# Performance work log

Hardware: AMD Instinct MI355X
Metric: run time of the kernel (lower is better)

Reference implementation:

```python
import jax, jax.numpy as jnp
import numpy as np

K = 5          # reassembly kernel size
S = 2          # scale factor
ENC_PAD = 1    # encoder_kernel_size // 2


def _conv2d(x, w, pad):
    return jax.lax.conv_general_dilated(
        x, w, window_strides=(1, 1), padding=[(pad, pad), (pad, pad)],
        dimension_numbers=('NCHW', 'OIHW', 'NCHW'))


def setup_inputs() -> dict:
    key = jax.random.key(0)
    k1, k2, k3 = jax.random.split(key, 3)
    x = jax.random.normal(k1, (2, 256, 40, 40), dtype=jnp.float32)
    # channel compressor: xavier-uniform-ish 1x1 conv weight (64, 256, 1, 1)
    limit = np.sqrt(6.0 / (256 + 64)).astype(np.float32)
    w_comp = jax.random.uniform(k2, (64, 256, 1, 1), dtype=jnp.float32,
                                minval=-limit, maxval=limit)
    # content encoder: normal(0, 0.001), out = k^2*s^2 = 100 channels
    w_enc = 0.001 * jax.random.normal(k3, (100, 64, 3, 3), dtype=jnp.float32)
    return {"x": x, "w_comp": w_comp, "w_enc": w_enc}


def reference(x, w_comp, w_enc):
    b, c, h, w = x.shape
    k2 = K * K
    h_up, w_up = h * S, w * S

    # --- kernel prediction ---
    compressed = _conv2d(x, w_comp, 0)                # (b, 64, h, w)
    kern = _conv2d(compressed, w_enc, ENC_PAD)        # (b, k2*S^2, h, w)
    # pixel shuffle: (b, k2, S, S, h, w) -> (b, k2, h, S, w, S) -> (b, k2, h_up, w_up)
    kern = kern.reshape(b, k2, S, S, h, w).transpose(0, 1, 4, 2, 5, 3)
    kern = kern.reshape(b, k2, h_up * w_up)
    kern = jax.nn.softmax(kern, axis=1)               # softmax over k2

    # --- unfold (im2col, padding K//2) ---
    pad = K // 2
    xp = jnp.pad(x, ((0, 0), (0, 0), (pad, pad), (pad, pad)))
    # (b, c, k2, h, w): channel-major, kernel offsets inner (matches torch F.unfold)
    patches = jnp.stack([xp[:, :, i:i + h, j:j + w]
                         for i in range(K) for j in range(K)], axis=2)
    x_unfold = patches.reshape(b, c, k2, h * w)

    # --- reassembly (faithful to the torch 'efficient' path) ---
    # torch repeat_interleaves x_unfold S^2 times along the h*w axis and
    # multiplies with kernels flattened in (h_up*w_up) row-major order; that
    # pairing is exactly kern reshaped to (b, k2, h*w, S^2):
    kern4 = kern.reshape(b, k2, h * w, S * S)
    out = jnp.einsum('bckp,bkpd->bcpd', x_unfold, kern4)  # (b, c, h*w, S^2)
    return out.reshape(b, c, h_up, w_up)
```

## Files before the change

### kernel.cpp

```cpp
#include <hip/hip_runtime.h>

#define B   2
#define C   256
#define CM  64
#define CE  100
#define H   40
#define W   40
#define HW  1600
#define KK  25

__global__ __launch_bounds__(256) void k1_conv1x1(
    const float* __restrict__ x, const float* __restrict__ w,
    float* __restrict__ pc) {
  const int t = blockIdx.x, ich = blockIdx.y, b = blockIdx.z;
  __shared__ __align__(16) float xs[64 * 64];
  __shared__ __align__(16) float wsA[64 * 64];
  const int tid = threadIdx.x;

  const float4* x4 = (const float4*)(x + ((size_t)b * C + ich * 64) * HW + t * 64);
#pragma unroll
  for (int i = 0; i < 4; i++) {
    int idx = tid + i * 256;
    ((float4*)xs)[idx] = x4[(idx >> 4) * 400 + (idx & 15)];
  }
  const float4* w4 = (const float4*)w;
#pragma unroll
  for (int i = 0; i < 4; i++) {
    int idx = tid + i * 256;
    int icq = idx >> 6, oc = idx & 63;
    float4 f = w4[oc * 64 + ich * 16 + icq];
    wsA[(icq * 4 + 0) * 64 + oc] = f.x;
    wsA[(icq * 4 + 1) * 64 + oc] = f.y;
    wsA[(icq * 4 + 2) * 64 + oc] = f.z;
    wsA[(icq * 4 + 3) * 64 + oc] = f.w;
  }
  __syncthreads();

  const int ty = tid >> 4, tx = tid & 15;
  float acc[4][4];
#pragma unroll
  for (int i = 0; i < 4; i++)
#pragma unroll
    for (int j = 0; j < 4; j++) acc[i][j] = 0.f;

#pragma unroll 4
  for (int icl = 0; icl < 64; icl++) {
    float4 a = *(const float4*)&wsA[icl * 64 + ty * 4];
    float4 bb = *(const float4*)&xs[icl * 64 + tx * 4];
    float av[4] = {a.x, a.y, a.z, a.w};
    float bv[4] = {bb.x, bb.y, bb.z, bb.w};
#pragma unroll
    for (int i = 0; i < 4; i++)
#pragma unroll
      for (int j = 0; j < 4; j++) acc[i][j] += av[i] * bv[j];
  }

  float* o = pc + ((size_t)ich * B + b) * CM * HW + t * 64 + tx * 4;
#pragma unroll
  for (int j = 0; j < 4; j++)
    *(float4*)&o[(size_t)(ty * 4 + j) * HW] =
        make_float4(acc[j][0], acc[j][1], acc[j][2], acc[j][3]);
}

__global__ __launch_bounds__(256) void k2_conv3x3(
    const float* __restrict__ pc, const float* __restrict__ w,
    float* __restrict__ encP) {
  const int tile = blockIdx.x, ocq = blockIdx.y, icq = blockIdx.z;
  const int ty5 = tile / 5, tx5 = tile % 5;
  __shared__ __align__(16) float smem[3200 + 16 * 9 * 28];
  float* cs  = smem;
  float* wsb = smem + 3200;
  float* pacc = smem;
  const int tid = threadIdx.x;

  for (int i = tid; i < 3200; i += 256) {
    int bb = i / 1600, r = i - bb * 1600;
    int icl = r / 100, rr = r - icl * 100;
    int yy = rr / 10, xx = rr - yy * 10;
    int gy = ty5 * 8 + yy - 1, gx = tx5 * 8 + xx - 1;
    float v = 0.f;
    if (gy >= 0 && gy < H && gx >= 0 && gx < W) {
      int o = bb * 102400 + (icq * 16 + icl) * HW + gy * W + gx;
      v = pc[o] + pc[204800 + o] + pc[409600 + o] + pc[614400 + o];
    }
    cs[i] = v;
  }
  const float* wb = w + (size_t)(ocq * 25) * 576 + (size_t)(icq * 16) * 9;
  for (int i = tid; i < 3600; i += 256) {
    int ol = i / 144, r = i - ol * 144;
    wsb[r * 28 + ol] = wb[ol * 576 + r];
  }
  __syncthreads();

  const int wv = tid >> 6, lane = tid & 63, py = lane >> 3, px = lane & 7;
  float acc[50];
#pragma unroll
  for (int j = 0; j < 50; j++) acc[j] = 0.f;

#pragma unroll 1
  for (int t = 0; t < 4; t++) {
    const int icl = wv * 4 + t;
    const float* c0 = &cs[icl * 100 + py * 10 + px];
    const float* c1 = c0 + 1600;
    const float* wrow = &wsb[icl * 9 * 28];
#pragma unroll
    for (int dy = 0; dy < 3; dy++) {
#pragma unroll
      for (int dx = 0; dx < 3; dx++) {
        float x0 = c0[dy * 10 + dx];
        float x1 = c1[dy * 10 + dx];
        const float* wp = &wrow[(dy * 3 + dx) * 28];
        float4 w0 = *(const float4*)&wp[0],  w1 = *(const float4*)&wp[4];
        float4 w2 = *(const float4*)&wp[8],  w3 = *(const float4*)&wp[12];
        float4 w4v = *(const float4*)&wp[16], w5 = *(const float4*)&wp[20];
        float w6 = wp[24];
        acc[0]  += x0 * w0.x;  acc[1]  += x0 * w0.y;  acc[2]  += x0 * w0.z;  acc[3]  += x0 * w0.w;
        acc[4]  += x0 * w1.x;  acc[5]  += x0 * w1.y;  acc[6]  += x0 * w1.z;  acc[7]  += x0 * w1.w;
        acc[8]  += x0 * w2.x;  acc[9]  += x0 * w2.y;  acc[10] += x0 * w2.z;  acc[11] += x0 * w2.w;
        acc[12] += x0 * w3.x;  acc[13] += x0 * w3.y;  acc[14] += x0 * w3.z;  acc[15] += x0 * w3.w;
        acc[16] += x0 * w4v.x; acc[17] += x0 * w4v.y; acc[18] += x0 * w4v.z; acc[19] += x0 * w4v.w;
        acc[20] += x0 * w5.x;  acc[21] += x0 * w5.y;  acc[22] += x0 * w5.z;  acc[23] += x0 * w5.w;
        acc[24] += x0 * w6;
        acc[25] += x1 * w0.x;  acc[26] += x1 * w0.y;  acc[27] += x1 * w0.z;  acc[28] += x1 * w0.w;
        acc[29] += x1 * w1.x;  acc[30] += x1 * w1.y;  acc[31] += x1 * w1.z;  acc[32] += x1 * w1.w;
        acc[33] += x1 * w2.x;  acc[34] += x1 * w2.y;  acc[35] += x1 * w2.z;  acc[36] += x1 * w2.w;
        acc[37] += x1 * w3.x;  acc[38] += x1 * w3.y;  acc[39] += x1 * w3.z;  acc[40] += x1 * w3.w;
        acc[41] += x1 * w4v.x; acc[42] += x1 * w4v.y; acc[43] += x1 * w4v.z; acc[44] += x1 * w4v.w;
        acc[45] += x1 * w5.x;  acc[46] += x1 * w5.y;  acc[47] += x1 * w5.z;  acc[48] += x1 * w5.w;
        acc[49] += x1 * w6;
      }
    }
  }

  __syncthreads();
  if (wv == 1 || wv == 3) {
    const int slot = wv >> 1;
#pragma unroll
    for (int j = 0; j < 50; j++) pacc[slot * 3200 + j * 64 + lane] = acc[j];
  }
  __syncthreads();
  if (wv == 0 || wv == 2) {
    const int slot = wv >> 1;
#pragma unroll
    for (int j = 0; j < 50; j++) acc[j] += pacc[slot * 3200 + j * 64 + lane];
  }
  __syncthreads();
  if (wv == 2) {
#pragma unroll
    for (int j = 0; j < 50; j++) pacc[j * 64 + lane] = acc[j];
  }
  __syncthreads();
  if (wv == 0) {
    const int base_px = (ty5 * 8 + py) * W + tx5 * 8 + px;
#pragma unroll
    for (int bb = 0; bb < 2; bb++)
#pragma unroll
      for (int ol = 0; ol < 25; ol++)
        encP[(((size_t)icq * 2 + bb) * CE + ocq * 25 + ol) * HW + base_px] =
            acc[bb * 25 + ol] + pacc[(bb * 25 + ol) * 64 + lane];
  }
}

__global__ __launch_bounds__(256) void k3_reassemble(
    const float* __restrict__ x, const float* __restrict__ encP,
    float* __restrict__ out) {
  const int i0 = blockIdx.x >> 1;
  const int jh = blockIdx.x & 1;
  const int cq = blockIdx.y;
  const int b = blockIdx.z;

  __shared__ __align__(16) float wlds[20 * KK * 4];
  __shared__ float xsm[64 * 121];

  const int tid = threadIdx.x;

  if (tid < 80) {
    const int e = jh * 80 + tid;
    const int j0 = e >> 2, d = e & 3;
    const int off = ((e >= 80) ? 2 : 0) + (e & 1);
    const int col = ((e >= 80) ? (j0 - 20) : j0) * 2 + (d >> 1);
    const float* ep = encP + (size_t)b * CE * HW + i0 * W + col;
    float v[KK];
    float m = -1e30f;
#pragma unroll
    for (int k = 0; k < KK; k++) {
      int o = (k * 4 + off) * HW;
      v[k] = ep[o] + ep[320000 + o] + ep[640000 + o] + ep[960000 + o];
      m = fmaxf(m, v[k]);
    }
    float s = 0.f;
#pragma unroll
    for (int k = 0; k < KK; k++) {
      v[k] = expf(v[k] - m);
      s += v[k];
    }
    const float inv = 1.f / s;
    const int j0l = j0 - jh * 20;
#pragma unroll
    for (int k = 0; k < KK; k++) wlds[(j0l * KK + k) * 4 + d] = v[k] * inv;
  }

  const float* xb = x + ((size_t)b * C + cq * 64) * HW;
  for (int i = tid; i < 64 * 120; i += 256) {
    int c = i / 120;
    int rr = i % 120;
    int r = rr / 24, t = rr % 24;
    int gy = i0 - 2 + r;
    int gx = jh * 20 + t - 2;
    float v = 0.f;
    if (gy >= 0 && gy < H && gx >= 0 && gx < W) v = xb[c * HW + gy * W + gx];
    xsm[c * 121 + r * 24 + t] = v;
  }
  __syncthreads();

  const int wv = tid >> 6;
  const int lane = tid & 63;
  float* ob = out + (((size_t)b * C + cq * 64 + lane) * 6400) + i0 * 160;
  const float* xrow = &xsm[lane * 121];
#pragma unroll 1
  for (int jj = 0; jj < 5; jj++) {
    const int j0l = wv * 5 + jj;
    const int j0 = jh * 20 + j0l;
    float a0 = 0.f, a1 = 0.f, a2 = 0.f, a3 = 0.f;
#pragma unroll
    for (int ki = 0; ki < 5; ki++) {
#pragma unroll
      for (int kj = 0; kj < 5; kj++) {
        float xv = xrow[ki * 24 + j0l + kj];
        float4 w4 = *(const float4*)&wlds[(j0l * KK + ki * 5 + kj) * 4];
        a0 += xv * w4.x;
        a1 += xv * w4.y;
        a2 += xv * w4.z;
        a3 += xv * w4.w;
      }
    }
    float4 o = make_float4(a0, a1, a2, a3);
    *(float4*)&ob[j0 * 4] = o;
  }
}

extern "C" void kernel_launch(void* const* d_in, const int* in_sizes, int n_in,
                              void* d_out, int out_size, void* d_ws, size_t ws_size,
                              hipStream_t stream) {
  const float* x      = (const float*)d_in[0];
  const float* w_comp = (const float*)d_in[1];
  const float* w_enc  = (const float*)d_in[2];
  float* out = (float*)d_out;

  float* pc   = (float*)d_ws;
  float* encP = (float*)((char*)d_ws + 3276800);

  k1_conv1x1<<<dim3(25, 4, B), 256, 0, stream>>>(x, w_comp, pc);
  k2_conv3x3<<<dim3(25, 4, 4), 256, 0, stream>>>(pc, w_enc, encP);
  k3_reassemble<<<dim3(80, 4, B), 256, 0, stream>>>(x, encP, out);
}
```

Baseline: 110.3 us.

## Process two output rows per block in reassembly kernel with register-blocked inputs

The reassembly kernel now computes two low-res output rows per block instead of one. The 6-row input halo is shared between them in LDS, so each block loads 6 input rows rather than 2×5 for two separate blocks. The inner loop loads a 9-element window of x into registers once per kernel row and reuses it across five adjacent output columns, which cuts LDS reads. The grid is halved to 320 blocks, which may reduce latency hiding on a GPU with many CUs, and the larger accumulator array adds register pressure.

```diff
diff --git a/kernel.cpp b/kernel.cpp
--- a/kernel.cpp
+++ b/kernel.cpp
@@ -164,22 +164,24 @@
 __global__ __launch_bounds__(256) void k3_reassemble(
     const float* __restrict__ x, const float* __restrict__ encP,
     float* __restrict__ out) {
-  const int i0 = blockIdx.x >> 1;
+  const int ib = blockIdx.x >> 1;
   const int jh = blockIdx.x & 1;
   const int cq = blockIdx.y;
   const int b = blockIdx.z;
 
-  __shared__ __align__(16) float wlds[20 * KK * 4];
-  __shared__ float xsm[64 * 121];
+  __shared__ __align__(16) float wlds[2 * 20 * KK * 4];
+  __shared__ float xsm[64 * 145];
 
   const int tid = threadIdx.x;
 
-  if (tid < 80) {
-    const int e = jh * 80 + tid;
-    const int j0 = e >> 2, d = e & 3;
-    const int off = ((e >= 80) ? 2 : 0) + (e & 1);
-    const int col = ((e >= 80) ? (j0 - 20) : j0) * 2 + (d >> 1);
-    const float* ep = encP + (size_t)b * CE * HW + i0 * W + col;
+  if (tid < 160) {
+    const int i0l = tid / 80;
+    const int rem = tid - i0l * 80;
+    const int j0l = rem >> 2, d = rem & 3;
+    const int i0 = 2 * ib + i0l;
+    const int off = jh * 2 + (d & 1);
+    const int colw = j0l * 2 + (d >> 1);
+    const float* ep = encP + (size_t)b * CE * HW + i0 * W + colw;
     float v[KK];
     float m = -1e30f;
 #pragma unroll
@@ -195,47 +197,62 @@
       s += v[k];
     }
     const float inv = 1.f / s;
-    const int j0l = j0 - jh * 20;
-#pragma unroll
-    for (int k = 0; k < KK; k++) wlds[(j0l * KK + k) * 4 + d] = v[k] * inv;
+#pragma unroll
+    for (int k = 0; k < KK; k++)
+      wlds[((i0l * 20 + j0l) * KK + k) * 4 + d] = v[k] * inv;
   }
 
   const float* xb = x + ((size_t)b * C + cq * 64) * HW;
-  for (int i = tid; i < 64 * 120; i += 256) {
-    int c = i / 120;
-    int rr = i % 120;
-    int r = rr / 24, t = rr % 24;
-    int gy = i0 - 2 + r;
+  for (int i = tid; i < 64 * 144; i += 256) {
+    int c = i / 144;
+    int rr = i - c * 144;
+    int r = rr / 24, t = rr - r * 24;
+    int gy = 2 * ib - 2 + r;
     int gx = jh * 20 + t - 2;
     float v = 0.f;
     if (gy >= 0 && gy < H && gx >= 0 && gx < W) v = xb[c * HW + gy * W + gx];
-    xsm[c * 121 + r * 24 + t] = v;
+    xsm[c * 145 + r * 24 + t] = v;
   }
   __syncthreads();
 
   const int wv = tid >> 6;
   const int lane = tid & 63;
-  float* ob = out + (((size_t)b * C + cq * 64 + lane) * 6400) + i0 * 160;
-  const float* xrow = &xsm[lane * 121];
+  const float* xrow = &xsm[lane * 145];
+  float* obase = out + (((size_t)b * C + cq * 64 + lane) * 6400) + jh * 80;
+
 #pragma unroll 1
-  for (int jj = 0; jj < 5; jj++) {
-    const int j0l = wv * 5 + jj;
-    const int j0 = jh * 20 + j0l;
-    float a0 = 0.f, a1 = 0.f, a2 = 0.f, a3 = 0.f;
+  for (int i0l = 0; i0l < 2; i0l++) {
+    float a[5][4];
+#pragma unroll
+    for (int jj = 0; jj < 5; jj++)
+#pragma unroll
+      for (int d = 0; d < 4; d++) a[jj][d] = 0.f;
+
 #pragma unroll
     for (int ki = 0; ki < 5; ki++) {
-#pragma unroll
-      for (int kj = 0; kj < 5; kj++) {
-        float xv = xrow[ki * 24 + j0l + kj];
-        float4 w4 = *(const float4*)&wlds[(j0l * KK + ki * 5 + kj) * 4];
-        a0 += xv * w4.x;
-        a1 += xv * w4.y;
-        a2 += xv * w4.z;
-        a3 += xv * w4.w;
+      float xv[9];
+      const float* xr = &xrow[(i0l + ki) * 24 + wv * 5];
+#pragma unroll
+      for (int q = 0; q < 9; q++) xv[q] = xr[q];
+      const float* wrow = &wlds[((i0l * 20 + wv * 5) * KK + ki * 5) * 4];
+#pragma unroll
+      for (int jj = 0; jj < 5; jj++) {
+#pragma unroll
+        for (int kj = 0; kj < 5; kj++) {
+          float4 w4 = *(const float4*)&wrow[(jj * KK + kj) * 4];
+          float xvv = xv[jj + kj];
+          a[jj][0] += xvv * w4.x;
+          a[jj][1] += xvv * w4.y;
+          a[jj][2] += xvv * w4.z;
+          a[jj][3] += xvv * w4.w;
+        }
       }
     }
-    float4 o = make_float4(a0, a1, a2, a3);
-    *(float4*)&ob[j0 * 4] = o;
+    float* ob = obase + (size_t)(2 * ib + i0l) * 160;
+#pragma unroll
+    for (int jj = 0; jj < 5; jj++)
+      *(float4*)&ob[(wv * 5 + jj) * 4] =
+          make_float4(a[jj][0], a[jj][1], a[jj][2], a[jj][3]);
   }
 }
 
@@ -252,5 +269,5 @@
 
   k1_conv1x1<<<dim3(25, 4, B), 256, 0, stream>>>(x, w_comp, pc);
   k2_conv3x3<<<dim3(25, 4, 4), 256, 0, stream>>>(pc, w_enc, encP);
-  k3_reassemble<<<dim3(80, 4, B), 256, 0, stream>>>(x, encP, out);
-}
+  k3_reassemble<<<dim3(40, 4, B), 256, 0, stream>>>(x, encP, out);
+}
```

Result: slower. 114.5 us (+3.9%).
